# Optimization experiments

Hardware: AMD Instinct MI355X
Metric: run time of the kernel (lower is better)

Reference implementation:

```python
import jax, jax.numpy as jnp
import numpy as np

BN_EPS = 1e-5
LEAKY_SLOPE = 0.1


def setup_inputs() -> dict:
    key = jax.random.key(0)
    ks = jax.random.split(key, 4)
    b, c, h, w = 4, 64, 64, 64
    exemplar = jax.random.normal(ks[0], (b, c, h, w), dtype=jnp.float32)
    query = jax.random.normal(ks[1], (b, c, h, w), dtype=jnp.float32)
    W_lin = jax.random.normal(ks[2], (c, c), dtype=jnp.float32) * (1.0 / np.sqrt(c))
    W_conv = jax.random.normal(ks[3], (c, c, 3, 3), dtype=jnp.float32) * (1.0 / np.sqrt(c * 9))
    gamma = jnp.ones((c,), dtype=jnp.float32)
    beta = jnp.zeros((c,), dtype=jnp.float32)
    return {"exemplar": exemplar, "query": query, "W_lin": W_lin,
            "W_conv": W_conv, "gamma": gamma, "beta": beta}


def reference(exemplar, query, W_lin, W_conv, gamma, beta):
    b, c, h, w = exemplar.shape
    hw = h * w
    ex_flat = exemplar.reshape(b, c, hw)          # [b, C, hw]
    q_flat = query.reshape(b, c, hw)              # [b, C, hw]
    # linear_e on transposed exemplar: [b, hw, C] @ W_lin.T
    ex_l = jnp.einsum('bnc,oc->bno', ex_flat.transpose(0, 2, 1), W_lin)
    # affinity A: [b, hw, hw]
    A = jnp.einsum('bnc,bcm->bnm', ex_l, q_flat)
    # B = softmax(A^T, dim=1); C = softmax(A, dim=1)
    Bmat = jax.nn.softmax(A.transpose(0, 2, 1), axis=1)
    Cmat = jax.nn.softmax(A, axis=1)
    query_c = jnp.einsum('bcm,bmn->bcn', q_flat, Bmat)     # [b, C, hw]
    exemplar_c = jnp.einsum('bcm,bmn->bcn', ex_flat, Cmat)  # [b, C, hw]
    out_x = (exemplar_c + query_c).reshape(b, c, h, w) + exemplar + query
    # conv3x3 (no bias) -> batchnorm (training-mode batch stats) -> leaky relu
    y = jax.lax.conv_general_dilated(
        out_x, W_conv, window_strides=(1, 1), padding=[(1, 1), (1, 1)],
        dimension_numbers=('NCHW', 'OIHW', 'NCHW'))
    mean = jnp.mean(y, axis=(0, 2, 3), keepdims=True)
    var = jnp.mean((y - mean) ** 2, axis=(0, 2, 3), keepdims=True)
    y = (y - mean) * jax.lax.rsqrt(var + BN_EPS)
    y = y * gamma[None, :, None, None] + beta[None, :, None, None]
    return jnp.where(y > 0, y, LEAKY_SLOPE * y)
```

## Files before the change

kernel.cpp:

```cpp
#include <hip/hip_runtime.h>


typedef short bf16x8 __attribute__((ext_vector_type(8)));
typedef float f32x4 __attribute__((ext_vector_type(4)));
typedef unsigned int u32x4 __attribute__((ext_vector_type(4)));
typedef unsigned short ushort_t;
typedef ushort_t ushort8 __attribute__((ext_vector_type(8)));

#define HW 4096
#define NC 64
#define NB 4
#define RT_L2E 1.2011224087864498f

#define GLB(p) ((const __attribute__((address_space(1))) unsigned int*)(p))
#define LDSP(p) ((__attribute__((address_space(3))) unsigned int*)(p))

__device__ __forceinline__ ushort_t f2bf(float f) {
  unsigned u = __builtin_bit_cast(unsigned, f);
  unsigned r = u + 0x7FFFu + ((u >> 16) & 1u);
  return (ushort_t)(r >> 16);
}

__device__ __forceinline__ float bf2f(ushort_t u) {
  unsigned v = ((unsigned)u) << 16;
  return __builtin_bit_cast(float, v);
}

__device__ __forceinline__ float fast_exp2(float x) {
#if __has_builtin(__builtin_amdgcn_exp2f)
  return __builtin_amdgcn_exp2f(x);
#else
  return exp2f(x);
#endif
}

__device__ __forceinline__ unsigned cvt_pk_bf16(float lo, float hi) {
  unsigned r;
  asm("v_cvt_pk_bf16_f32 %0, %1, %2" : "=v"(r) : "v"(lo), "v"(hi));
  return r;
}

__global__ __launch_bounds__(256) void prep_kernel(
    const float* __restrict__ ex, const float* __restrict__ q,
    const float* __restrict__ Wl, const float* __restrict__ Wc,
    ushort_t* __restrict__ exlT_s, ushort_t* __restrict__ qT_s,
    ushort_t* __restrict__ q_tl, ushort_t* __restrict__ ex_tl,
    ushort_t* __restrict__ exq, ushort_t* __restrict__ w9f)
{
  __shared__ float exs[64][33];
  __shared__ float wls[64][64];

  const int t = threadIdx.x;
  const int b = blockIdx.x >> 7;
  const int chunk = blockIdx.x & 127;
  const int g = t >> 5;
  const int p = t & 31;
  const int pos = chunk * 32 + p;
  const int tile = pos >> 6;
  const int kv = pos & 63;
  const int vcol = ((kv >> 5) << 5) + (((kv >> 2) & 3) << 3)
                 + (((kv >> 4) & 1) << 2) + (kv & 3);

  {
    int widx = blockIdx.x * 256 + t;
    if (widx < 36864) {
      int o   = widx / 576;
      int rem = widx - o * 576;
      int c   = rem / 9;
      int tap = rem - c * 9;
      w9f[tap * 4096 + o * 64 + c] = f2bf(Wc[widx]);
    }
  }

  const float* exb = ex + (size_t)b * NC * HW;
  const float* qb  = q  + (size_t)b * NC * HW;
  ushort_t* exlTsb = exlT_s+ (size_t)b * HW * NC;
  ushort_t* qTsb   = qT_s  + (size_t)b * HW * NC;
  ushort_t* exqb   = exq   + (size_t)b * HW * NC;
  ushort_t* qtlb   = q_tl  + (size_t)b * HW * NC + (size_t)tile * 4096 + vcol;
  ushort_t* etlb   = ex_tl + (size_t)b * HW * NC + (size_t)tile * 4096 + vcol;

#pragma unroll
  for (int it = 0; it < 16; ++it) {
    int idx = it * 256 + t;
    wls[idx >> 6][idx & 63] = Wl[idx];
  }

  ushort8 qhs, eqh;
#pragma unroll
  for (int j = 0; j < 8; ++j) {
    int c = g * 8 + j;
    float ev = exb[c * HW + pos];
    exs[c][p] = ev;
    etlb[c * 64] = f2bf(ev);
    float qv = qb[c * HW + pos];
    qtlb[c * 64] = f2bf(qv);
    qhs[j] = f2bf(qv * RT_L2E);
    eqh[j] = f2bf(ev + qv);
  }
  *(ushort8*)(qTsb + (size_t)pos * NC + g * 8) = qhs;
  *(ushort8*)(exqb + (size_t)pos * NC + g * 8) = eqh;
  __syncthreads();

  float acc[8];
#pragma unroll
  for (int oo = 0; oo < 8; ++oo) acc[oo] = 0.f;
  for (int c = 0; c < 64; ++c) {
    float xv = exs[c][p];
#pragma unroll
    for (int oo = 0; oo < 8; ++oo)
      acc[oo] += wls[g * 8 + oo][c] * xv;
  }
  {
    ushort8 hs;
#pragma unroll
    for (int oo = 0; oo < 8; ++oo) hs[oo] = f2bf(acc[oo] * RT_L2E);
    *(ushort8*)(exlTsb + (size_t)pos * NC + g * 8) = hs;
  }
}

__global__ __launch_bounds__(512, 4) void attn_kernel(
    const ushort_t* __restrict__ exlT_s, const ushort_t* __restrict__ qT_s,
    const ushort_t* __restrict__ q_tl, const ushort_t* __restrict__ ex_tl,
    ushort_t* __restrict__ Opart, float* __restrict__ lpart, int ss)
{
  __shared__ char smem[65536];

  const int gid  = blockIdx.x;
  const int S    = 1 << ss;
  const int kvs  = gid & (S - 1);
  const int qb   = (gid >> ss) & 15;
  const int b    = (gid >> (ss + 4)) & 3;
  const int pass = gid >> (ss + 6);
  const int w    = threadIdx.x >> 6;
  const int lane = threadIdx.x & 63;
  const int lr = lane & 15, lg = lane >> 4;
  const int qrow0 = qb * 256 + w * 32;

  const ushort_t* QT = (pass ? qT_s : exlT_s) + (size_t)b * HW * NC;
  const ushort_t* KT = (pass ? exlT_s : qT_s) + (size_t)b * HW * NC;
  const ushort_t* VT = (pass ? ex_tl : q_tl) + (size_t)b * HW * NC;

  bf16x8 aq0[2], aq1[2];
  {
    const ushort_t* qp0 = QT + (size_t)(qrow0 + lr) * NC + lg * 8;
    aq0[0] = *(const bf16x8*)(qp0);
    aq0[1] = *(const bf16x8*)(qp0 + 32);
    const ushort_t* qp1 = QT + (size_t)(qrow0 + 16 + lr) * NC + lg * 8;
    aq1[0] = *(const bf16x8*)(qp1);
    aq1[1] = *(const bf16x8*)(qp1 + 32);
  }

  const u32x4 onesu = {0x3F803F80u, 0x3F803F80u, 0x3F803F80u, 0x3F803F80u};
  const bf16x8 vones = __builtin_bit_cast(bf16x8, onesu);

  f32x4 O0[4], O1[4];
  f32x4 lacc0 = (f32x4){0.f, 0.f, 0.f, 0.f};
  f32x4 lacc1 = (f32x4){0.f, 0.f, 0.f, 0.f};
#pragma unroll
  for (int t = 0; t < 4; ++t) {
    O0[t] = (f32x4){0.f, 0.f, 0.f, 0.f};
    O1[t] = (f32x4){0.f, 0.f, 0.f, 0.f};
  }

  const int niter = 64 >> ss;
  const int kv0 = kvs * niter;

  const int db0 = w * 1024 + (lane << 4);
#define STAGE(phase, kvb)                                                      \
  {                                                                            \
    char* Kl = smem + (phase) * 16384;                                         \
    char* Vl = Kl + 8192;                                                      \
    const char* kg = (const char*)(KT + (size_t)(kvb) * 64 * NC);              \
    const char* vg = (const char*)(VT + (size_t)(kvb) * 4096);                 \
    int swz = db0 ^ (((db0 >> 7) & 7) << 4);                                   \
    __builtin_amdgcn_global_load_lds(GLB(kg + swz),                            \
                                     LDSP(Kl + w * 1024), 16, 0, 0);           \
    __builtin_amdgcn_global_load_lds(GLB(vg + swz),                            \
                                     LDSP(Vl + w * 1024), 16, 0, 0);           \
  }

  STAGE(0, kv0);
  STAGE(1, kv0 + 1);
  __syncthreads();

  int pair = 0;
  for (int i = 0; i < niter; i += 2) {
    if (i + 2 < niter) {
      const int np = (pair ^ 1) * 2;
      STAGE(np, kv0 + i + 2);
      if (i + 3 < niter) STAGE(np + 1, kv0 + i + 3);
    }

    const int cswz = (lr & 7) << 4;

#pragma unroll
    for (int half = 0; half < 2; ++half) {
      const char* Kl = smem + (pair * 2 + half) * 16384;
      const char* Vl = Kl + 8192;

      f32x4 s0[4], s1[4];
#pragma unroll
      for (int t = 0; t < 4; ++t) {
        s0[t] = (f32x4){0.f, 0.f, 0.f, 0.f};
        s1[t] = (f32x4){0.f, 0.f, 0.f, 0.f};
      }
      __builtin_amdgcn_s_setprio(1);
#pragma unroll
      for (int ks = 0; ks < 2; ++ks)
#pragma unroll
        for (int t = 0; t < 4; ++t) {
          bf16x8 kf = *(const bf16x8*)(Kl + (t * 16 + lr) * 128
                                       + ((ks * 64 + lg * 16) ^ cswz));
          s0[t] = __builtin_amdgcn_mfma_f32_16x16x32_bf16(kf, aq0[ks], s0[t], 0, 0, 0);
          s1[t] = __builtin_amdgcn_mfma_f32_16x16x32_bf16(kf, aq1[ks], s1[t], 0, 0, 0);
        }
      __builtin_amdgcn_s_setprio(0);

      unsigned int pa0[2][4], pa1[2][4];
#pragma unroll
      for (int ks = 0; ks < 2; ++ks)
#pragma unroll
        for (int hf = 0; hf < 2; ++hf) {
          const int t = ks * 2 + hf;
          float a0 = fast_exp2(s0[t][0]);
          float a1 = fast_exp2(s0[t][1]);
          float a2 = fast_exp2(s0[t][2]);
          float a3 = fast_exp2(s0[t][3]);
          pa0[ks][hf * 2]     = cvt_pk_bf16(a0, a1);
          pa0[ks][hf * 2 + 1] = cvt_pk_bf16(a2, a3);
          float c0 = fast_exp2(s1[t][0]);
          float c1 = fast_exp2(s1[t][1]);
          float c2 = fast_exp2(s1[t][2]);
          float c3 = fast_exp2(s1[t][3]);
          pa1[ks][hf * 2]     = cvt_pk_bf16(c0, c1);
          pa1[ks][hf * 2 + 1] = cvt_pk_bf16(c2, c3);
        }

      __builtin_amdgcn_s_setprio(1);
#pragma unroll
      for (int ks = 0; ks < 2; ++ks) {
        u32x4 pv0 = {pa0[ks][0], pa0[ks][1], pa0[ks][2], pa0[ks][3]};
        u32x4 pv1 = {pa1[ks][0], pa1[ks][1], pa1[ks][2], pa1[ks][3]};
        bf16x8 paf0 = __builtin_bit_cast(bf16x8, pv0);
        bf16x8 paf1 = __builtin_bit_cast(bf16x8, pv1);
        lacc0 = __builtin_amdgcn_mfma_f32_16x16x32_bf16(paf0, vones, lacc0, 0, 0, 0);
        lacc1 = __builtin_amdgcn_mfma_f32_16x16x32_bf16(paf1, vones, lacc1, 0, 0, 0);
#pragma unroll
        for (int t = 0; t < 4; ++t) {
          bf16x8 vf = *(const bf16x8*)(Vl + (t * 16 + lr) * 128
                                       + ((ks * 64 + lg * 16) ^ cswz));
          O0[t] = __builtin_amdgcn_mfma_f32_16x16x32_bf16(paf0, vf, O0[t], 0, 0, 0);
          O1[t] = __builtin_amdgcn_mfma_f32_16x16x32_bf16(paf1, vf, O1[t], 0, 0, 0);
        }
      }
      __builtin_amdgcn_s_setprio(0);
    }

    __syncthreads();
    pair ^= 1;
  }

  ushort_t* Ob = Opart + ((size_t)((pass * 4 + b) * S + kvs)) * (HW * NC);
  float* lp = lpart + ((size_t)((pass * 4 + b) * S + kvs)) * HW;
#pragma unroll
  for (int t = 0; t < 4; ++t)
#pragma unroll
    for (int r = 0; r < 4; ++r) {
      Ob[(size_t)(qrow0 + lg * 4 + r) * NC + t * 16 + lr] = f2bf(O0[t][r]);
      Ob[(size_t)(qrow0 + 16 + lg * 4 + r) * NC + t * 16 + lr] = f2bf(O1[t][r]);
    }
  if (lr == 0) {
#pragma unroll
    for (int r = 0; r < 4; ++r) {
      lp[qrow0 + lg * 4 + r] = lacc0[r];
      lp[qrow0 + 16 + lg * 4 + r] = lacc1[r];
    }
  }
#undef STAGE
}

__global__ __launch_bounds__(256) void merge_kernel(
    const ushort_t* __restrict__ Opart, const float* __restrict__ lpart,
    const ushort_t* __restrict__ exq, ushort_t* __restrict__ xconv, int S)
{
  const int idx = blockIdx.x * 256 + threadIdx.x;
  const int c8  = (idx & 7) * 8;
  const int pos = (idx >> 3) & 4095;
  const int b   = idx >> 15;
  const int h   = pos >> 6;
  const int w   = pos & 63;

  float acc[8];
  {
    ushort8 e = *(const ushort8*)(exq + ((size_t)b * HW + pos) * NC + c8);
#pragma unroll
    for (int j = 0; j < 8; ++j) acc[j] = bf2f(e[j]);
  }

#pragma unroll
  for (int pass = 0; pass < 2; ++pass) {
    const int pp = pass * 4 + b;
    const ushort_t* opb = Opart + (size_t)pp * S * (HW * NC)
                        + (size_t)pos * NC + c8;
    float os[8];
#pragma unroll
    for (int j = 0; j < 8; ++j) os[j] = 0.f;
    float ls = 0.f;
    for (int s = 0; s < S; ++s) {
      ushort8 v = *(const ushort8*)(opb + (size_t)s * (HW * NC));
#pragma unroll
      for (int j = 0; j < 8; ++j) os[j] += bf2f(v[j]);
      ls += lpart[(size_t)(pp * S + s) * HW + pos];
    }
    float inv = 1.0f / ls;
#pragma unroll
    for (int j = 0; j < 8; ++j) acc[j] += os[j] * inv;
  }

  ushort_t* row = xconv + ((size_t)(b * 64 + h) * 66) * NC;
  ushort8 outv;
#pragma unroll
  for (int j = 0; j < 8; ++j) outv[j] = f2bf(acc[j]);
  *(ushort8*)(row + (size_t)(w + 1) * NC + c8) = outv;

  ushort8 z = {0, 0, 0, 0, 0, 0, 0, 0};
  if (w == 0)  *(ushort8*)(row + c8) = z;
  if (w == 63) *(ushort8*)(row + (size_t)65 * NC + c8) = z;
}

#define XSZ 25344
__global__ __launch_bounds__(256) void conv_kernel(
    const ushort_t* __restrict__ xconv, const ushort_t* __restrict__ w9f,
    float* __restrict__ y, float* __restrict__ pstats)
{
  __shared__ char smem[XSZ + 73728];
  const int t  = threadIdx.x;
  const int h  = blockIdx.x & 63;
  const int b  = blockIdx.x >> 6;
  const int wv = t >> 6;
  const int lane = t & 63;
  const int lr = lane & 15, lg = lane >> 4;

  {
    const char* wsrc = (const char*)w9f;
#pragma unroll
    for (int i = 0; i < 18; ++i) {
      int d = (i * 256 + t) * 16;
      int s = d ^ (((d >> 7) & 7) << 4);
      __builtin_amdgcn_global_load_lds(GLB(wsrc + s),
          LDSP(smem + XSZ + (i * 256 + wv * 64) * 16), 16, 0, 0);
    }
  }

#pragma unroll
  for (int ky = 0; ky < 3; ++ky) {
    const int hs = h + ky - 1;
    char* dst0 = smem + ky * 8448;
    if (hs >= 0 && hs < 64) {
      const char* src = (const char*)(xconv + (size_t)(b * 64 + hs) * 66 * NC);
#pragma unroll
      for (int i = 0; i < 2; ++i) {
        int d = (i * 256 + t) * 16;
        int s = d ^ (((d >> 7) & 7) << 4);
        __builtin_amdgcn_global_load_lds(GLB(src + s),
            LDSP(dst0 + (i * 256 + wv * 64) * 16), 16, 0, 0);
      }
      if (t < 16) {
        int d = (512 + t) * 16;
        int s = d ^ (((d >> 7) & 7) << 4);
        __builtin_amdgcn_global_load_lds(GLB(src + s),
            LDSP(dst0 + 512 * 16), 16, 0, 0);
      }
    } else {
      u32x4 z = {0, 0, 0, 0};
#pragma unroll
      for (int i = 0; i < 2; ++i)
        *(u32x4*)(dst0 + (i * 256 + t) * 16) = z;
      if (t < 16) *(u32x4*)(dst0 + (512 + t) * 16) = z;
    }
  }
  __syncthreads();

  const char* xls = smem;
  const char* wls = smem + XSZ;

  f32x4 O[4];
#pragma unroll
  for (int tt = 0; tt < 4; ++tt) O[tt] = (f32x4){0.f, 0.f, 0.f, 0.f};

  const int orow = wv * 16 + lr;
  const int oswz = (lr & 7) << 4;

#pragma unroll
  for (int tap = 0; tap < 9; ++tap) {
    const int ky = tap / 3, kx = tap % 3;
    bf16x8 wa[2];
#pragma unroll
    for (int ks = 0; ks < 2; ++ks)
      wa[ks] = *(const bf16x8*)(wls + tap * 8192 + orow * 128
                                + (((ks * 4 + lg) << 4) ^ oswz));
#pragma unroll
    for (int tt = 0; tt < 4; ++tt) {
      const int row = tt * 16 + lr + kx;
      const int rswz = (row & 7) << 4;
#pragma unroll
      for (int ks = 0; ks < 2; ++ks) {
        bf16x8 bf = *(const bf16x8*)(xls + ky * 8448 + row * 128
                                     + (((ks * 4 + lg) << 4) ^ rswz));
        O[tt] = __builtin_amdgcn_mfma_f32_16x16x32_bf16(wa[ks], bf, O[tt], 0, 0, 0);
      }
    }
  }

  float* ps = pstats + (size_t)blockIdx.x * 128;
#pragma unroll
  for (int r = 0; r < 4; ++r) {
    const int o = wv * 16 + lg * 4 + r;
    float s1 = 0.f, s2 = 0.f;
#pragma unroll
    for (int tt = 0; tt < 4; ++tt) {
      float v = O[tt][r];
      y[(size_t)(b * 64 + o) * HW + h * 64 + tt * 16 + lr] = v;
      s1 += v; s2 += v * v;
    }
    s1 += __shfl_xor(s1, 1); s1 += __shfl_xor(s1, 2);
    s1 += __shfl_xor(s1, 4); s1 += __shfl_xor(s1, 8);
    s2 += __shfl_xor(s2, 1); s2 += __shfl_xor(s2, 2);
    s2 += __shfl_xor(s2, 4); s2 += __shfl_xor(s2, 8);
    if (lr == 0) { ps[o] = s1; ps[64 + o] = s2; }
  }
}

__global__ __launch_bounds__(128) void statred_kernel(
    const float* __restrict__ pstats, float* __restrict__ stats)
{
  const int i = threadIdx.x;
  float s = 0.f;
  for (int k = 0; k < 256; ++k) s += pstats[k * 128 + i];
  stats[i] = s;
}

__global__ __launch_bounds__(256) void bn_kernel(
    const float* __restrict__ y, const float* __restrict__ stats,
    const float* __restrict__ gamma, const float* __restrict__ beta,
    float* __restrict__ out)
{
  const int e = (blockIdx.x * 256 + threadIdx.x) * 4;
  const int o = (e >> 12) & 63;
  float mean = stats[o] * (1.f / 16384.f);
  float var  = stats[64 + o] * (1.f / 16384.f) - mean * mean;
  float g  = gamma[o] * rsqrtf(var + 1e-5f);
  float bt = beta[o] - mean * g;
  float4 v = *(const float4*)(y + e);
  float4 r;
  r.x = v.x * g + bt; r.x = r.x > 0.f ? r.x : 0.1f * r.x;
  r.y = v.y * g + bt; r.y = r.y > 0.f ? r.y : 0.1f * r.y;
  r.z = v.z * g + bt; r.z = r.z > 0.f ? r.z : 0.1f * r.z;
  r.w = v.w * g + bt; r.w = r.w > 0.f ? r.w : 0.1f * r.w;
  *(float4*)(out + e) = r;
}

extern "C" void kernel_launch(void* const* d_in, const int* in_sizes, int n_in,
                              void* d_out, int out_size, void* d_ws, size_t ws_size,
                              hipStream_t stream)
{
  const float* ex    = (const float*)d_in[0];
  const float* q     = (const float*)d_in[1];
  const float* Wl    = (const float*)d_in[2];
  const float* Wc    = (const float*)d_in[3];
  const float* gamma = (const float*)d_in[4];
  const float* beta  = (const float*)d_in[5];
  float* out = (float*)d_out;

  char* ws = (char*)d_ws;
  ushort_t* exlT_s = (ushort_t*)(ws);
  ushort_t* qT_s   = (ushort_t*)(ws + (2u << 20));
  ushort_t* q_tl   = (ushort_t*)(ws + (4u << 20));
  ushort_t* ex_tl  = (ushort_t*)(ws + (6u << 20));
  ushort_t* exq    = (ushort_t*)(ws + (8u << 20));
  ushort_t* xconv  = (ushort_t*)(ws + (10u << 20));
  float* stats  = (float*)(ws + (14u << 20));
  float* lpart  = (float*)(ws + (14u << 20) + 65536);
  float* pstats = (float*)(ws + (14u << 20) + 589824);
  ushort_t* w9f = (ushort_t*)(ws + (14u << 20) + 786432);
  ushort_t* Opart = (ushort_t*)(ws + (15u << 20));
  float* yBuf  = (float*)(ws);

  int ss;
  if (ws_size >= (31u << 20)) ss = 2;
  else if (ws_size >= (23u << 20)) ss = 1;
  else ss = 0;
  const int S = 1 << ss;

  prep_kernel<<<512, 256, 0, stream>>>(ex, q, Wl, Wc, exlT_s, qT_s, q_tl, ex_tl,
                                       exq, w9f);
  attn_kernel<<<128 * S, 512, 0, stream>>>(exlT_s, qT_s, q_tl, ex_tl,
                                           Opart, lpart, ss);
  merge_kernel<<<512, 256, 0, stream>>>(Opart, lpart, exq, xconv, S);
  conv_kernel<<<256, 256, 0, stream>>>(xconv, w9f, yBuf, pstats);
  statred_kernel<<<1, 128, 0, stream>>>(pstats, stats);
  bn_kernel<<<1024, 256, 0, stream>>>(yBuf, stats, gamma, beta, out);
}
```

Before: 67.87 us.

## Split conv work across output-channel halves and widen stat reduction

The conv kernel now launches twice as many blocks, each covering half the output channels for one row. Each of its 8 waves computes a single 16x16 tile instead of four, which spreads the conv over more CUs and loads only half the weights per block. The per-block partial stats grow to 2048 entries, with zeros written for the unused half, so the stat reduction kernel now uses 1024 threads and reduces through shared memory. The cost is that each input row is loaded twice, and pstats moves to a new workspace offset that must not overlap other buffers.

```diff
diff --git a/kernel.cpp b/kernel.cpp
--- a/kernel.cpp
+++ b/kernel.cpp
@@ -330,26 +330,35 @@
 }
 
 #define XSZ 25344
-__global__ __launch_bounds__(256) void conv_kernel(
+__global__ __launch_bounds__(512) void conv_kernel(
     const ushort_t* __restrict__ xconv, const ushort_t* __restrict__ w9f,
     float* __restrict__ y, float* __restrict__ pstats)
 {
-  __shared__ char smem[XSZ + 73728];
+  __shared__ char smem[XSZ + 36864];
   const int t  = threadIdx.x;
-  const int h  = blockIdx.x & 63;
-  const int b  = blockIdx.x >> 6;
-  const int wv = t >> 6;
+  const int oh = blockIdx.x & 1;
+  const int h  = (blockIdx.x >> 1) & 63;
+  const int b  = blockIdx.x >> 7;
+  const int w8 = t >> 6;
   const int lane = t & 63;
   const int lr = lane & 15, lg = lane >> 4;
+  const int oq = w8 >> 2;
+  const int wq = w8 & 3;
 
   {
-    const char* wsrc = (const char*)w9f;
-#pragma unroll
-    for (int i = 0; i < 18; ++i) {
-      int d = (i * 256 + t) * 16;
-      int s = d ^ (((d >> 7) & 7) << 4);
-      __builtin_amdgcn_global_load_lds(GLB(wsrc + s),
-          LDSP(smem + XSZ + (i * 256 + wv * 64) * 16), 16, 0, 0);
+#pragma unroll
+    for (int i = 0; i < 5; ++i) {
+      int idx = i * 512 + t;
+      if (idx < 2304) {
+        int d    = idx * 16;
+        int tap  = d >> 12;
+        int rem  = d & 4095;
+        int orow = rem >> 7;
+        int col  = (rem & 127) ^ ((orow & 7) << 4);
+        int src  = tap * 8192 + (oh * 32 + orow) * 128 + col;
+        __builtin_amdgcn_global_load_lds(GLB((const char*)w9f + src),
+            LDSP(smem + XSZ + (i * 512 + w8 * 64) * 16), 16, 0, 0);
+      }
     }
   }
 
@@ -359,12 +368,11 @@
     char* dst0 = smem + ky * 8448;
     if (hs >= 0 && hs < 64) {
       const char* src = (const char*)(xconv + (size_t)(b * 64 + hs) * 66 * NC);
-#pragma unroll
-      for (int i = 0; i < 2; ++i) {
-        int d = (i * 256 + t) * 16;
+      {
+        int d = t * 16;
         int s = d ^ (((d >> 7) & 7) << 4);
         __builtin_amdgcn_global_load_lds(GLB(src + s),
-            LDSP(dst0 + (i * 256 + wv * 64) * 16), 16, 0, 0);
+            LDSP(dst0 + w8 * 1024), 16, 0, 0);
       }
       if (t < 16) {
         int d = (512 + t) * 16;
@@ -374,9 +382,7 @@
       }
     } else {
       u32x4 z = {0, 0, 0, 0};
-#pragma unroll
-      for (int i = 0; i < 2; ++i)
-        *(u32x4*)(dst0 + (i * 256 + t) * 16) = z;
+      *(u32x4*)(dst0 + t * 16) = z;
       if (t < 16) *(u32x4*)(dst0 + (512 + t) * 16) = z;
     }
   }
@@ -385,60 +391,61 @@
   const char* xls = smem;
   const char* wls = smem + XSZ;
 
-  f32x4 O[4];
-#pragma unroll
-  for (int tt = 0; tt < 4; ++tt) O[tt] = (f32x4){0.f, 0.f, 0.f, 0.f};
-
-  const int orow = wv * 16 + lr;
-  const int oswz = (lr & 7) << 4;
+  f32x4 O = (f32x4){0.f, 0.f, 0.f, 0.f};
+  const int aswz = (lr & 7) << 4;
 
 #pragma unroll
   for (int tap = 0; tap < 9; ++tap) {
-    const int ky = tap / 3, kx = tap % 3;
-    bf16x8 wa[2];
-#pragma unroll
-    for (int ks = 0; ks < 2; ++ks)
-      wa[ks] = *(const bf16x8*)(wls + tap * 8192 + orow * 128
-                                + (((ks * 4 + lg) << 4) ^ oswz));
-#pragma unroll
-    for (int tt = 0; tt < 4; ++tt) {
-      const int row = tt * 16 + lr + kx;
-      const int rswz = (row & 7) << 4;
-#pragma unroll
-      for (int ks = 0; ks < 2; ++ks) {
-        bf16x8 bf = *(const bf16x8*)(xls + ky * 8448 + row * 128
-                                     + (((ks * 4 + lg) << 4) ^ rswz));
-        O[tt] = __builtin_amdgcn_mfma_f32_16x16x32_bf16(wa[ks], bf, O[tt], 0, 0, 0);
-      }
-    }
-  }
-
-  float* ps = pstats + (size_t)blockIdx.x * 128;
+    const int kyy = tap / 3, kx = tap % 3;
+    const int brow = wq * 16 + lr + kx;
+    const int bswz = (brow & 7) << 4;
+#pragma unroll
+    for (int ks = 0; ks < 2; ++ks) {
+      bf16x8 wa = *(const bf16x8*)(wls + tap * 4096 + (oq * 16 + lr) * 128
+                                   + (((ks * 4 + lg) << 4) ^ aswz));
+      bf16x8 bf = *(const bf16x8*)(xls + kyy * 8448 + brow * 128
+                                   + (((ks * 4 + lg) << 4) ^ bswz));
+      O = __builtin_amdgcn_mfma_f32_16x16x32_bf16(wa, bf, O, 0, 0, 0);
+    }
+  }
+
+  float* ps = pstats + ((size_t)blockIdx.x * 4 + wq) * 128;
 #pragma unroll
   for (int r = 0; r < 4; ++r) {
-    const int o = wv * 16 + lg * 4 + r;
-    float s1 = 0.f, s2 = 0.f;
-#pragma unroll
-    for (int tt = 0; tt < 4; ++tt) {
-      float v = O[tt][r];
-      y[(size_t)(b * 64 + o) * HW + h * 64 + tt * 16 + lr] = v;
-      s1 += v; s2 += v * v;
-    }
+    const int o = oh * 32 + oq * 16 + lg * 4 + r;
+    float v = O[r];
+    y[(size_t)(b * 64 + o) * HW + h * 64 + wq * 16 + lr] = v;
+    float s1 = v, s2 = v * v;
     s1 += __shfl_xor(s1, 1); s1 += __shfl_xor(s1, 2);
     s1 += __shfl_xor(s1, 4); s1 += __shfl_xor(s1, 8);
     s2 += __shfl_xor(s2, 1); s2 += __shfl_xor(s2, 2);
     s2 += __shfl_xor(s2, 4); s2 += __shfl_xor(s2, 8);
-    if (lr == 0) { ps[o] = s1; ps[64 + o] = s2; }
-  }
-}
-
-__global__ __launch_bounds__(128) void statred_kernel(
+    if (lr == 0) {
+      ps[o] = s1; ps[64 + o] = s2;
+      const int om = o ^ 32;
+      ps[om] = 0.f; ps[64 + om] = 0.f;
+    }
+  }
+}
+
+__global__ __launch_bounds__(1024) void statred_kernel(
     const float* __restrict__ pstats, float* __restrict__ stats)
 {
-  const int i = threadIdx.x;
+  __shared__ float red[8][128];
+  const int tid = threadIdx.x;
+  const int i = tid & 127;
+  const int chunk = tid >> 7;
   float s = 0.f;
-  for (int k = 0; k < 256; ++k) s += pstats[k * 128 + i];
-  stats[i] = s;
+  for (int k = 0; k < 256; ++k)
+    s += pstats[(size_t)(chunk * 256 + k) * 128 + i];
+  red[chunk][i] = s;
+  __syncthreads();
+  if (tid < 128) {
+    float r = 0.f;
+#pragma unroll
+    for (int c = 0; c < 8; ++c) r += red[c][tid];
+    stats[tid] = r;
+  }
 }
 
 __global__ __launch_bounds__(256) void bn_kernel(
@@ -480,9 +487,9 @@
   ushort_t* ex_tl  = (ushort_t*)(ws + (6u << 20));
   ushort_t* exq    = (ushort_t*)(ws + (8u << 20));
   ushort_t* xconv  = (ushort_t*)(ws + (10u << 20));
+  float* pstats = (float*)(ws + 13107200u);
   float* stats  = (float*)(ws + (14u << 20));
   float* lpart  = (float*)(ws + (14u << 20) + 65536);
-  float* pstats = (float*)(ws + (14u << 20) + 589824);
   ushort_t* w9f = (ushort_t*)(ws + (14u << 20) + 786432);
   ushort_t* Opart = (ushort_t*)(ws + (15u << 20));
   float* yBuf  = (float*)(ws);
@@ -498,7 +505,7 @@
   attn_kernel<<<128 * S, 512, 0, stream>>>(exlT_s, qT_s, q_tl, ex_tl,
                                            Opart, lpart, ss);
   merge_kernel<<<512, 256, 0, stream>>>(Opart, lpart, exq, xconv, S);
-  conv_kernel<<<256, 256, 0, stream>>>(xconv, w9f, yBuf, pstats);
-  statred_kernel<<<1, 128, 0, stream>>>(pstats, stats);
+  conv_kernel<<<512, 512, 0, stream>>>(xconv, w9f, yBuf, pstats);
+  statred_kernel<<<1, 1024, 0, stream>>>(pstats, stats);
   bn_kernel<<<1024, 256, 0, stream>>>(yBuf, stats, gamma, beta, out);
 }
```

After: 73.65 us. 8.5% more time.

## Interleave two KV tiles per iteration and compute row sums with VALU adds

Applied to the files above, without the earlier changes.

The inner loop now computes the QK^T scores for both staged KV tiles up front, then does exp and PV for each tile in turn, so the second tile's score MFMAs can overlap the first tile's exponentials. The softmax denominator, previously accumulated with an extra MFMA against a ones vector, is now summed in fp32 registers and reduced across lane groups with shuffles once at the end. This removes four MFMAs per tile and sums unrounded fp32 values instead of bf16-rounded ones. In exchange it adds VALU adds and raises register pressure from holding two sets of score accumulators.

```diff
diff --git a/kernel.cpp b/kernel.cpp
--- a/kernel.cpp
+++ b/kernel.cpp
@@ -151,12 +151,8 @@
     aq1[1] = *(const bf16x8*)(qp1 + 32);
   }
 
-  const u32x4 onesu = {0x3F803F80u, 0x3F803F80u, 0x3F803F80u, 0x3F803F80u};
-  const bf16x8 vones = __builtin_bit_cast(bf16x8, onesu);
-
   f32x4 O0[4], O1[4];
-  f32x4 lacc0 = (f32x4){0.f, 0.f, 0.f, 0.f};
-  f32x4 lacc1 = (f32x4){0.f, 0.f, 0.f, 0.f};
+  float lsum0 = 0.f, lsum1 = 0.f;
 #pragma unroll
   for (int t = 0; t < 4; ++t) {
     O0[t] = (f32x4){0.f, 0.f, 0.f, 0.f};
@@ -193,73 +189,126 @@
     }
 
     const int cswz = (lr & 7) << 4;
-
-#pragma unroll
-    for (int half = 0; half < 2; ++half) {
-      const char* Kl = smem + (pair * 2 + half) * 16384;
-      const char* Vl = Kl + 8192;
-
-      f32x4 s0[4], s1[4];
+    const char* KlA = smem + (pair * 2) * 16384;
+    const char* VlA = KlA + 8192;
+    const char* KlB = KlA + 16384;
+    const char* VlB = KlB + 8192;
+
+    f32x4 sA0[4], sA1[4], sB0[4], sB1[4];
+#pragma unroll
+    for (int t = 0; t < 4; ++t) {
+      sA0[t] = (f32x4){0.f, 0.f, 0.f, 0.f};
+      sA1[t] = (f32x4){0.f, 0.f, 0.f, 0.f};
+      sB0[t] = (f32x4){0.f, 0.f, 0.f, 0.f};
+      sB1[t] = (f32x4){0.f, 0.f, 0.f, 0.f};
+    }
+    __builtin_amdgcn_s_setprio(1);
+#pragma unroll
+    for (int ks = 0; ks < 2; ++ks)
 #pragma unroll
       for (int t = 0; t < 4; ++t) {
-        s0[t] = (f32x4){0.f, 0.f, 0.f, 0.f};
-        s1[t] = (f32x4){0.f, 0.f, 0.f, 0.f};
-      }
-      __builtin_amdgcn_s_setprio(1);
-#pragma unroll
-      for (int ks = 0; ks < 2; ++ks)
-#pragma unroll
-        for (int t = 0; t < 4; ++t) {
-          bf16x8 kf = *(const bf16x8*)(Kl + (t * 16 + lr) * 128
-                                       + ((ks * 64 + lg * 16) ^ cswz));
-          s0[t] = __builtin_amdgcn_mfma_f32_16x16x32_bf16(kf, aq0[ks], s0[t], 0, 0, 0);
-          s1[t] = __builtin_amdgcn_mfma_f32_16x16x32_bf16(kf, aq1[ks], s1[t], 0, 0, 0);
-        }
-      __builtin_amdgcn_s_setprio(0);
-
-      unsigned int pa0[2][4], pa1[2][4];
-#pragma unroll
-      for (int ks = 0; ks < 2; ++ks)
-#pragma unroll
-        for (int hf = 0; hf < 2; ++hf) {
-          const int t = ks * 2 + hf;
-          float a0 = fast_exp2(s0[t][0]);
-          float a1 = fast_exp2(s0[t][1]);
-          float a2 = fast_exp2(s0[t][2]);
-          float a3 = fast_exp2(s0[t][3]);
-          pa0[ks][hf * 2]     = cvt_pk_bf16(a0, a1);
-          pa0[ks][hf * 2 + 1] = cvt_pk_bf16(a2, a3);
-          float c0 = fast_exp2(s1[t][0]);
-          float c1 = fast_exp2(s1[t][1]);
-          float c2 = fast_exp2(s1[t][2]);
-          float c3 = fast_exp2(s1[t][3]);
-          pa1[ks][hf * 2]     = cvt_pk_bf16(c0, c1);
-          pa1[ks][hf * 2 + 1] = cvt_pk_bf16(c2, c3);
-        }
-
-      __builtin_amdgcn_s_setprio(1);
-#pragma unroll
-      for (int ks = 0; ks < 2; ++ks) {
-        u32x4 pv0 = {pa0[ks][0], pa0[ks][1], pa0[ks][2], pa0[ks][3]};
-        u32x4 pv1 = {pa1[ks][0], pa1[ks][1], pa1[ks][2], pa1[ks][3]};
-        bf16x8 paf0 = __builtin_bit_cast(bf16x8, pv0);
-        bf16x8 paf1 = __builtin_bit_cast(bf16x8, pv1);
-        lacc0 = __builtin_amdgcn_mfma_f32_16x16x32_bf16(paf0, vones, lacc0, 0, 0, 0);
-        lacc1 = __builtin_amdgcn_mfma_f32_16x16x32_bf16(paf1, vones, lacc1, 0, 0, 0);
-#pragma unroll
-        for (int t = 0; t < 4; ++t) {
-          bf16x8 vf = *(const bf16x8*)(Vl + (t * 16 + lr) * 128
-                                       + ((ks * 64 + lg * 16) ^ cswz));
-          O0[t] = __builtin_amdgcn_mfma_f32_16x16x32_bf16(paf0, vf, O0[t], 0, 0, 0);
-          O1[t] = __builtin_amdgcn_mfma_f32_16x16x32_bf16(paf1, vf, O1[t], 0, 0, 0);
-        }
-      }
-      __builtin_amdgcn_s_setprio(0);
-    }
+        bf16x8 kf = *(const bf16x8*)(KlA + (t * 16 + lr) * 128
+                                     + ((ks * 64 + lg * 16) ^ cswz));
+        sA0[t] = __builtin_amdgcn_mfma_f32_16x16x32_bf16(kf, aq0[ks], sA0[t], 0, 0, 0);
+        sA1[t] = __builtin_amdgcn_mfma_f32_16x16x32_bf16(kf, aq1[ks], sA1[t], 0, 0, 0);
+      }
+#pragma unroll
+    for (int ks = 0; ks < 2; ++ks)
+#pragma unroll
+      for (int t = 0; t < 4; ++t) {
+        bf16x8 kf = *(const bf16x8*)(KlB + (t * 16 + lr) * 128
+                                     + ((ks * 64 + lg * 16) ^ cswz));
+        sB0[t] = __builtin_amdgcn_mfma_f32_16x16x32_bf16(kf, aq0[ks], sB0[t], 0, 0, 0);
+        sB1[t] = __builtin_amdgcn_mfma_f32_16x16x32_bf16(kf, aq1[ks], sB1[t], 0, 0, 0);
+      }
+    __builtin_amdgcn_s_setprio(0);
+
+    unsigned int paA0[2][4], paA1[2][4];
+#pragma unroll
+    for (int ks = 0; ks < 2; ++ks)
+#pragma unroll
+      for (int hf = 0; hf < 2; ++hf) {
+        const int t = ks * 2 + hf;
+        float a0 = fast_exp2(sA0[t][0]);
+        float a1 = fast_exp2(sA0[t][1]);
+        float a2 = fast_exp2(sA0[t][2]);
+        float a3 = fast_exp2(sA0[t][3]);
+        lsum0 += (a0 + a1) + (a2 + a3);
+        paA0[ks][hf * 2]     = cvt_pk_bf16(a0, a1);
+        paA0[ks][hf * 2 + 1] = cvt_pk_bf16(a2, a3);
+        float c0 = fast_exp2(sA1[t][0]);
+        float c1 = fast_exp2(sA1[t][1]);
+        float c2 = fast_exp2(sA1[t][2]);
+        float c3 = fast_exp2(sA1[t][3]);
+        lsum1 += (c0 + c1) + (c2 + c3);
+        paA1[ks][hf * 2]     = cvt_pk_bf16(c0, c1);
+        paA1[ks][hf * 2 + 1] = cvt_pk_bf16(c2, c3);
+      }
+
+    __builtin_amdgcn_s_setprio(1);
+#pragma unroll
+    for (int ks = 0; ks < 2; ++ks) {
+      u32x4 pv0 = {paA0[ks][0], paA0[ks][1], paA0[ks][2], paA0[ks][3]};
+      u32x4 pv1 = {paA1[ks][0], paA1[ks][1], paA1[ks][2], paA1[ks][3]};
+      bf16x8 paf0 = __builtin_bit_cast(bf16x8, pv0);
+      bf16x8 paf1 = __builtin_bit_cast(bf16x8, pv1);
+#pragma unroll
+      for (int t = 0; t < 4; ++t) {
+        bf16x8 vf = *(const bf16x8*)(VlA + (t * 16 + lr) * 128
+                                     + ((ks * 64 + lg * 16) ^ cswz));
+        O0[t] = __builtin_amdgcn_mfma_f32_16x16x32_bf16(paf0, vf, O0[t], 0, 0, 0);
+        O1[t] = __builtin_amdgcn_mfma_f32_16x16x32_bf16(paf1, vf, O1[t], 0, 0, 0);
+      }
+    }
+    __builtin_amdgcn_s_setprio(0);
+
+    unsigned int paB0[2][4], paB1[2][4];
+#pragma unroll
+    for (int ks = 0; ks < 2; ++ks)
+#pragma unroll
+      for (int hf = 0; hf < 2; ++hf) {
+        const int t = ks * 2 + hf;
+        float a0 = fast_exp2(sB0[t][0]);
+        float a1 = fast_exp2(sB0[t][1]);
+        float a2 = fast_exp2(sB0[t][2]);
+        float a3 = fast_exp2(sB0[t][3]);
+        lsum0 += (a0 + a1) + (a2 + a3);
+        paB0[ks][hf * 2]     = cvt_pk_bf16(a0, a1);
+        paB0[ks][hf * 2 + 1] = cvt_pk_bf16(a2, a3);
+        float c0 = fast_exp2(sB1[t][0]);
+        float c1 = fast_exp2(sB1[t][1]);
+        float c2 = fast_exp2(sB1[t][2]);
+        float c3 = fast_exp2(sB1[t][3]);
+        lsum1 += (c0 + c1) + (c2 + c3);
+        paB1[ks][hf * 2]     = cvt_pk_bf16(c0, c1);
+        paB1[ks][hf * 2 + 1] = cvt_pk_bf16(c2, c3);
+      }
+
+    __builtin_amdgcn_s_setprio(1);
+#pragma unroll
+    for (int ks = 0; ks < 2; ++ks) {
+      u32x4 pv0 = {paB0[ks][0], paB0[ks][1], paB0[ks][2], paB0[ks][3]};
+      u32x4 pv1 = {paB1[ks][0], paB1[ks][1], paB1[ks][2], paB1[ks][3]};
+      bf16x8 paf0 = __builtin_bit_cast(bf16x8, pv0);
+      bf16x8 paf1 = __builtin_bit_cast(bf16x8, pv1);
+#pragma unroll
+      for (int t = 0; t < 4; ++t) {
+        bf16x8 vf = *(const bf16x8*)(VlB + (t * 16 + lr) * 128
+                                     + ((ks * 64 + lg * 16) ^ cswz));
+        O0[t] = __builtin_amdgcn_mfma_f32_16x16x32_bf16(paf0, vf, O0[t], 0, 0, 0);
+        O1[t] = __builtin_amdgcn_mfma_f32_16x16x32_bf16(paf1, vf, O1[t], 0, 0, 0);
+      }
+    }
+    __builtin_amdgcn_s_setprio(0);
 
     __syncthreads();
     pair ^= 1;
   }
+
+  lsum0 += __shfl_xor(lsum0, 16);
+  lsum0 += __shfl_xor(lsum0, 32);
+  lsum1 += __shfl_xor(lsum1, 16);
+  lsum1 += __shfl_xor(lsum1, 32);
 
   ushort_t* Ob = Opart + ((size_t)((pass * 4 + b) * S + kvs)) * (HW * NC);
   float* lp = lpart + ((size_t)((pass * 4 + b) * S + kvs)) * HW;
@@ -270,12 +319,9 @@
       Ob[(size_t)(qrow0 + lg * 4 + r) * NC + t * 16 + lr] = f2bf(O0[t][r]);
       Ob[(size_t)(qrow0 + 16 + lg * 4 + r) * NC + t * 16 + lr] = f2bf(O1[t][r]);
     }
-  if (lr == 0) {
-#pragma unroll
-    for (int r = 0; r < 4; ++r) {
-      lp[qrow0 + lg * 4 + r] = lacc0[r];
-      lp[qrow0 + 16 + lg * 4 + r] = lacc1[r];
-    }
+  if (lane < 16) {
+    lp[qrow0 + lane] = lsum0;
+    lp[qrow0 + 16 + lane] = lsum1;
   }
 #undef STAGE
 }
```

New measurement: 89.82 us. 32.3% more time.
